# Kernel optimization log

Hardware: AMD Instinct MI355X
Metric: run time of the kernel (lower is better)

Reference implementation:

```python
import jax, jax.numpy as jnp
import numpy as np

B, P, K_NN, HEADS = 4, 2048, 30, 3
N = B * P


def knn_nbr(feat):
    """Per-cloud exact KNN (no self), returns [N, K_NN+1] global neighbor idx, self appended last.
    Matches torch_geometric knn_graph (loop=False) followed by GATConv add_self_loops=True."""
    f = feat.reshape(B, P, -1)
    sq = jnp.sum(f * f, axis=-1)  # [B,P]
    d = sq[:, :, None] + sq[:, None, :] - 2.0 * jnp.einsum('bpc,bqc->bpq', f, f)
    d = d + jnp.eye(P, dtype=f.dtype)[None] * 1e9  # exclude self
    idx = jax.lax.top_k(-d, K_NN)[1]  # [B,P,K_NN] nearest neighbors
    idx = (idx + (jnp.arange(B) * P)[:, None, None]).reshape(N, K_NN)
    return jnp.concatenate([idx, jnp.arange(N)[:, None]], axis=1)  # self-loop last


def gat(xf, nbr, W, a_src, a_dst, bias):
    """PyG GATConv (v1, concat=True, negative_slope=0.2). nbr: [N,K] incoming sources per node."""
    H, F = a_src.shape
    xh = (xf @ W).reshape(N, H, F)
    s = jnp.sum(xh * a_src, axis=-1)  # [N,H] source scores
    t = jnp.sum(xh * a_dst, axis=-1)  # [N,H] target scores
    e = jax.nn.leaky_relu(s[nbr] + t[:, None, :], 0.2)  # [N,K,H]
    alpha = jax.nn.softmax(e, axis=1)  # edge-softmax over incoming edges
    out = jnp.einsum('nkh,nkhf->nhf', alpha, xh[nbr])
    return out.reshape(N, H * F) + bias


def setup_inputs() -> dict:
    key = jax.random.key(0)
    ks = jax.random.split(key, 48)
    w = lambda k, shape: (jax.random.normal(k, shape, jnp.float32) * 0.1)
    H = HEADS
    inp = {
        'x': jax.random.normal(ks[0], (N, 3), jnp.float32),
        'pos': jax.random.normal(ks[1], (N, 3), jnp.float32),
        'batch': (jnp.arange(N) // P).astype(jnp.int32),
        'w1': w(ks[2], (6, 64 * H)), 'as1': w(ks[3], (H, 64)), 'ad1': w(ks[4], (H, 64)), 'b1': w(ks[5], (64 * H,)),
        'ml1w': w(ks[6], (64 * H, 64)), 'ml1b': w(ks[7], (64,)),
        'w2': w(ks[8], (70, 64 * H)), 'as2': w(ks[9], (H, 64)), 'ad2': w(ks[10], (H, 64)), 'b2': w(ks[11], (64 * H,)),
        'ml2w': w(ks[12], (64 * H, 64)), 'ml2b': w(ks[13], (64,)),
        'w3': w(ks[14], (134, 64 * H)), 'as3': w(ks[15], (H, 64)), 'ad3': w(ks[16], (H, 64)), 'b3': w(ks[17], (64 * H,)),
        'ml3w': w(ks[18], (64 * H, 64)), 'ml3b': w(ks[19], (64,)),
        'w4': w(ks[20], (198, 128 * H)), 'as4': w(ks[21], (H, 128)), 'ad4': w(ks[22], (H, 128)), 'b4': w(ks[23], (128 * H,)),
        'ml4w': w(ks[24], (128 * H, 128)), 'ml4b': w(ks[25], (128,)),
        # fe_mlp: 326 -> 1024 -> 1024 (plain last)
        'few1': w(ks[26], (326, 1024)), 'feb1': w(ks[27], (1024,)),
        'few2': w(ks[28], (1024, 1024)), 'feb2': w(ks[29], (1024,)),
        # head mlp: 1350 -> 256 -> 256 -> 128 -> 50
        'mw1': w(ks[30], (1350, 256)), 'mb1': w(ks[31], (256,)),
        'mw2': w(ks[32], (256, 256)), 'mb2': w(ks[33], (256,)),
        'mw3': w(ks[34], (256, 128)), 'mb3': w(ks[35], (128,)),
        'mw4': w(ks[36], (128, 50)), 'mb4': w(ks[37], (50,)),
    }
    return inp


def reference(x, pos, batch,
              w1, as1, ad1, b1, ml1w, ml1b,
              w2, as2, ad2, b2, ml2w, ml2b,
              w3, as3, ad3, b3, ml3w, ml3b,
              w4, as4, ad4, b4, ml4w, ml4b,
              few1, feb1, few2, feb2,
              mw1, mb1, mw2, mb2, mw3, mb3, mw4, mb4):
    x0 = jnp.concatenate([x, pos], axis=-1)  # [N,6]
    nbr = knn_nbr(x0)
    x1 = gat(x0, nbr, w1, as1, ad1, b1) @ ml1w + ml1b  # [N,64]
    nbr = knn_nbr(x1)
    x2 = gat(jnp.concatenate([x0, x1], 1), nbr, w2, as2, ad2, b2) @ ml2w + ml2b
    nbr = knn_nbr(x2)
    x3 = gat(jnp.concatenate([x0, x1, x2], 1), nbr, w3, as3, ad3, b3) @ ml3w + ml3b
    nbr = knn_nbr(x2)  # faithful to source: 4th graph also built from x2
    x4 = gat(jnp.concatenate([x0, x1, x2, x3], 1), nbr, w4, as4, ad4, b4) @ ml4w + ml4b
    link4 = jnp.concatenate([x0, x1, x2, x3, x4], axis=-1)  # [N,326]
    h = jax.nn.relu(link4 @ few1 + feb1) @ few2 + feb2  # [N,1024]
    g = jnp.max(h, axis=0, keepdims=True)  # global feature (dropout=eval identity)
    lg = jnp.concatenate([link4, jnp.broadcast_to(g, (N, h.shape[1]))], axis=1)
    h = jax.nn.relu(lg @ mw1 + mb1)
    h = jax.nn.relu(h @ mw2 + mb2)
    h = jax.nn.relu(h @ mw3 + mb3)
    out = h @ mw4 + mb4
    return jax.nn.log_softmax(out, axis=1)
```

## Files before the change

### kernel.cpp

```cpp
#include <hip/hip_runtime.h>
#include <hip/hip_bf16.h>
#include <hip/amd_detail/amd_hip_vector_types.h>

#define NPTS 8192
#define PP 2048
#define KNN 30
#define KTOT 31
#define HEADS 3
#define LDH 352
#define NSEG 9
#define LDZ 200
#define LDZ4 392

typedef __attribute__((ext_vector_type(8))) short short8;
typedef __attribute__((ext_vector_type(4))) float floatx4;
typedef __attribute__((ext_vector_type(4))) unsigned int uint4_t;
typedef unsigned short ushort_t;
typedef unsigned int uint_t;

__device__ inline ushort_t f2bs(float v) {
    __hip_bfloat16 b = __float2bfloat16(v);
    return *reinterpret_cast<ushort_t*>(&b);
}
__device__ inline float bs2f(ushort_t u) {
    __hip_bfloat16 b = *reinterpret_cast<__hip_bfloat16*>(&u);
    return __bfloat162float(b);
}
__device__ inline void split2(float v, ushort_t& h, ushort_t& l) {
    h = f2bs(v);
    l = f2bs(v - bs2f(h));
}
__device__ inline uint_t fenc(float f) {
    uint_t b = __float_as_uint(f);
    return (b & 0x80000000u) ? ~b : (b | 0x80000000u);
}
__device__ inline float fdec(uint_t e) {
    return __uint_as_float((e & 0x80000000u) ? (e & 0x7FFFFFFFu) : ~e);
}

__global__ void k_build_x0(const float* __restrict__ x, const float* __restrict__ pos,
                           ushort_t* __restrict__ lh, ushort_t* __restrict__ ll) {
    int i = blockIdx.x * blockDim.x + threadIdx.x;
    if (i >= NPTS * 6) return;
    int n = i / 6, c = i % 6;
    float v = (c < 3) ? x[n * 3 + c] : pos[n * 3 + (c - 3)];
    ushort_t h, l; split2(v, h, l);
    lh[(size_t)n * LDH + c] = h;
    ll[(size_t)n * LDH + c] = l;
}

template<int F_>
__global__ __launch_bounds__(128)
void k_combine(const float* __restrict__ w, const float* __restrict__ mlw,
               const float* __restrict__ as_, const float* __restrict__ ad,
               const float* __restrict__ b, const float* __restrict__ mlb,
               float* __restrict__ wc, float* __restrict__ bc, int K_) {
    constexpr int NC = 3 * F_ + 6;
    constexpr int JG = 128 / F_;
    constexpr int RG = 8 / JG;
    int lb = blockIdx.x;
    int h = lb % 3, kb = lb / 3;
    int k0 = kb * 8, KS = min(8, K_ - k0);
    int tid = threadIdx.x;
    int j = tid % F_, rg = tid / F_;
    __shared__ float ws[8][F_];
    __shared__ float ms[32][F_];
    __shared__ float bav[3][F_];
    for (int idx = tid; idx < 8 * F_; idx += 128) {
        int r = idx / F_, f = idx % F_;
        ws[r][f] = (r < KS) ? w[(size_t)(k0 + r) * (3 * F_) + h * F_ + f] : 0.f;
    }
    for (int f = tid; f < F_; f += 128) {
        bav[0][f] = b[h * F_ + f];
        bav[1][f] = as_[h * F_ + f];
        bav[2][f] = ad[h * F_ + f];
    }
    __syncthreads();
    const float* mh = mlw + (size_t)h * F_ * F_;
    float acc[RG] = {};
    float bacc = 0.f;
    for (int f0 = 0; f0 < F_; f0 += 32) {
        for (int idx = tid; idx < 32 * F_; idx += 128) {
            int u = idx / F_, jj = idx % F_;
            ms[u][jj] = mh[(size_t)(f0 + u) * F_ + jj];
        }
        __syncthreads();
#pragma unroll
        for (int u = 0; u < 32; u++) {
            float m = ms[u][j];
#pragma unroll
            for (int r = 0; r < RG; r++)
                acc[r] += ws[rg * RG + r][f0 + u] * m;
            if (rg == 0) bacc += bav[0][f0 + u] * m;
        }
        __syncthreads();
    }
#pragma unroll
    for (int r = 0; r < RG; r++) {
        int k = k0 + rg * RG + r;
        if (k < K_) wc[(size_t)k * NC + h * F_ + j] = acc[r];
    }
    if (kb == 0 && rg == 0)
        atomicAdd(&bc[j], bacc + (h == 0 ? mlb[j] : 0.f));
    if (tid < 16) {
        int r = tid >> 1, sc = tid & 1;
        if (r < KS) {
            float s = 0.f;
#pragma unroll
            for (int f = 0; f < F_; f++) s += ws[r][f] * bav[1 + sc][f];
            wc[(size_t)(k0 + r) * NC + 3 * F_ + sc * 3 + h] = s;
        }
    }
}

__global__ void k_tw1(const float* __restrict__ x, const float* __restrict__ pos,
                      const float* __restrict__ wc, float* __restrict__ z) {
    int t = blockIdx.x * blockDim.x + threadIdx.x;
    if (t >= NPTS * 198) return;
    int n = t / 198, j = t % 198;
    float acc = 0.f;
#pragma unroll
    for (int c = 0; c < 3; c++) {
        acc += x[n * 3 + c] * wc[c * 198 + j];
        acc += pos[n * 3 + c] * wc[(3 + c) * 198 + j];
    }
    z[(size_t)n * LDZ + j] = acc;
}

struct WArgs {
    const float* src[NSEG];
    ushort_t* dst[NSEG];
    int K[NSEG], N[NSEG], Kp[NSEG], t0[NSEG];
};
__global__ void k_wsplit_all(WArgs a) {
    int bt = blockIdx.x;
    int si = 0;
#pragma unroll
    for (int i = 1; i < NSEG; i++) if (bt >= a.t0[i]) si = i;
    int t = bt - a.t0[si];
    int K_ = a.K[si], N_ = a.N[si], Kp = a.Kp[si];
    const float* src = a.src[si];
    ushort_t* dh = a.dst[si];
    ushort_t* dl = dh + (size_t)Kp * N_;
    int tX = (N_ + 31) >> 5;
    int k0 = (t / tX) * 32, n0 = (t % tX) * 32;
    __shared__ float tt[32][33];
    int c = threadIdx.x & 31, r8 = threadIdx.x >> 5;
#pragma unroll
    for (int i = 0; i < 4; i++) {
        int r = r8 + i * 8;
        int k = k0 + r, n = n0 + c;
        tt[r][c] = (k < K_ && n < N_) ? src[(size_t)k * N_ + n] : 0.f;
    }
    __syncthreads();
#pragma unroll
    for (int i = 0; i < 4; i++) {
        int r = r8 + i * 8;
        int n = n0 + r, k = k0 + c;
        if (n < N_) {
            float v = tt[c][r];
            ushort_t h, l; split2(v, h, l);
            dh[(size_t)n * Kp + k] = h;
            dl[(size_t)n * Kp + k] = l;
        }
    }
}

template<int MT, int NT>
__global__ __launch_bounds__(256)
void k_mgemm1(const ushort_t* __restrict__ A, int lda,
              const ushort_t* __restrict__ W, int ldw,
              float* __restrict__ Cf, int ldc,
              ushort_t* __restrict__ Ch, int ldh,
              int Ndim, int K,
              const float* __restrict__ bias1, const float* __restrict__ bias2,
              int relu, int lsm, uint_t* __restrict__ gmax) {
    constexpr int MTW = MT / 64;
    constexpr int NTT = NT / 16;
    __shared__ ushort_t As[2][MT * 40];
    __shared__ ushort_t Bs[2][NT * 40];
    __shared__ uint_t smax[NT];
    int tid = threadIdx.x;
    int w = tid >> 6, lane = tid & 63;
    int quad = lane >> 4, l16 = lane & 15;
    int m0 = blockIdx.x * MT, n0 = blockIdx.y * NT;
    uint4_t pa[MT / 64], pb[NT / 64];
    auto prefetch = [&](int k0) {
#pragma unroll
        for (int rep = 0; rep < MT / 64; rep++) {
            int idx = tid + rep * 256;
            int row = idx >> 2, q = idx & 3;
            pa[rep] = *(const uint4_t*)(A + (size_t)(m0 + row) * lda + k0 + q * 8);
        }
#pragma unroll
        for (int rep = 0; rep < NT / 64; rep++) {
            int idx = tid + rep * 256;
            int row = idx >> 2, q = idx & 3;
            uint4_t v = {0, 0, 0, 0};
            if (n0 + row < Ndim) v = *(const uint4_t*)(W + (size_t)(n0 + row) * ldw + k0 + q * 8);
            pb[rep] = v;
        }
    };
    auto stage = [&](int buf) {
#pragma unroll
        for (int rep = 0; rep < MT / 64; rep++) {
            int idx = tid + rep * 256;
            int row = idx >> 2, q = idx & 3;
            *(uint4_t*)&As[buf][row * 40 + q * 8] = pa[rep];
        }
#pragma unroll
        for (int rep = 0; rep < NT / 64; rep++) {
            int idx = tid + rep * 256;
            int row = idx >> 2, q = idx & 3;
            *(uint4_t*)&Bs[buf][row * 40 + q * 8] = pb[rep];
        }
    };
    if (gmax) {
        for (int idx = tid; idx < NT; idx += 256) smax[idx] = 0u;
    }
    floatx4 acc[MTW][NTT] = {};
    prefetch(0);
    stage(0);
    __syncthreads();
    int cur = 0;
    for (int k0 = 0; k0 < K; k0 += 32) {
        bool more = (k0 + 32 < K);
        if (more) prefetch(k0 + 32);
        short8 ah[MTW];
#pragma unroll
        for (int mt = 0; mt < MTW; mt++) {
            int r = w * (MT / 4) + mt * 16 + l16;
            ah[mt] = *(short8*)&As[cur][r * 40 + quad * 8];
        }
#pragma unroll
        for (int nt = 0; nt < NTT; nt++) {
            int r = nt * 16 + l16;
            short8 bh = *(short8*)&Bs[cur][r * 40 + quad * 8];
#pragma unroll
            for (int mt = 0; mt < MTW; mt++)
                acc[mt][nt] = __builtin_amdgcn_mfma_f32_16x16x32_bf16(ah[mt], bh, acc[mt][nt], 0, 0, 0);
        }
        if (more) stage(cur ^ 1);
        __syncthreads();
        cur ^= 1;
    }
    if (lsm) {
#pragma unroll
        for (int mt = 0; mt < MTW; mt++) {
#pragma unroll
            for (int r = 0; r < 4; r++) {
                float vv[NTT];
                float mrow = -3e38f;
#pragma unroll
                for (int nt = 0; nt < NTT; nt++) {
                    int n = n0 + nt * 16 + l16;
                    float val = (n < Ndim) ? acc[mt][nt][r] + bias1[n] : -3e38f;
                    vv[nt] = val;
                    mrow = fmaxf(mrow, val);
                }
#pragma unroll
                for (int off = 8; off >= 1; off >>= 1)
                    mrow = fmaxf(mrow, __shfl_xor(mrow, off, 64));
                float s = 0.f;
#pragma unroll
                for (int nt = 0; nt < NTT; nt++)
                    if (vv[nt] > -1e38f) s += expf(vv[nt] - mrow);
#pragma unroll
                for (int off = 8; off >= 1; off >>= 1)
                    s += __shfl_xor(s, off, 64);
                float lse = mrow + logf(s);
                int m = m0 + w * (MT / 4) + mt * 16 + quad * 4 + r;
#pragma unroll
                for (int nt = 0; nt < NTT; nt++) {
                    int n = n0 + nt * 16 + l16;
                    if (n < Ndim) Cf[(size_t)m * ldc + n] = vv[nt] - lse;
                }
            }
        }
        return;
    }
    if (gmax) {
#pragma unroll
        for (int mt = 0; mt < MTW; mt++) {
#pragma unroll
            for (int nt = 0; nt < NTT; nt++) {
#pragma unroll
                for (int r = 0; r < 4; r++) {
                    float v = acc[mt][nt][r] + bias1[nt * 16 + l16 + n0];
                    atomicMax(&smax[nt * 16 + l16], fenc(v));
                }
            }
        }
        __syncthreads();
        for (int idx = tid; idx < NT; idx += 256)
            atomicMax(&gmax[n0 + idx], smax[idx]);
        return;
    }
#pragma unroll
    for (int mt = 0; mt < MTW; mt++) {
#pragma unroll
        for (int nt = 0; nt < NTT; nt++) {
#pragma unroll
            for (int r = 0; r < 4; r++) {
                int m = m0 + w * (MT / 4) + mt * 16 + quad * 4 + r;
                int n = n0 + nt * 16 + l16;
                if (n < Ndim) {
                    float v = acc[mt][nt][r];
                    if (bias1) v += bias1[n];
                    if (bias2) v += bias2[n];
                    if (relu && v < 0.f) v = 0.f;
                    if (Cf) Cf[(size_t)m * ldc + n] = v;
                    if (Ch) Ch[(size_t)m * ldh + n] = f2bs(v);
                }
            }
        }
    }
}

__global__ __launch_bounds__(256)
void k_mgemm3(const ushort_t* __restrict__ Ah, const ushort_t* __restrict__ Al, int lda,
              const ushort_t* __restrict__ Wh, const ushort_t* __restrict__ Wl, int ldw,
              float* __restrict__ Cf, int ldc,
              int Ndim, int K) {
    constexpr int NTT = 4;
    __shared__ ushort_t AsH[64 * 40], BsH[64 * 40], AsL[64 * 40], BsL[64 * 40];
    int tid = threadIdx.x;
    int w = tid >> 6, lane = tid & 63;
    int quad = lane >> 4, l16 = lane & 15;
    int m0 = blockIdx.y * 64, n0 = blockIdx.x * 64;
    floatx4 acc[NTT] = {};
    for (int k0 = 0; k0 < K; k0 += 32) {
        {
            int row = tid >> 2, q = tid & 3;
            size_t go = (size_t)(m0 + row) * lda + k0 + q * 8;
            *(uint4_t*)&AsH[row * 40 + q * 8] = *(const uint4_t*)(Ah + go);
            *(uint4_t*)&AsL[row * 40 + q * 8] = *(const uint4_t*)(Al + go);
            uint4_t vh = {0, 0, 0, 0}, vl = {0, 0, 0, 0};
            size_t gw = (size_t)(n0 + row) * ldw + k0 + q * 8;
            if (n0 + row < Ndim) { vh = *(const uint4_t*)(Wh + gw); vl = *(const uint4_t*)(Wl + gw); }
            *(uint4_t*)&BsH[row * 40 + q * 8] = vh;
            *(uint4_t*)&BsL[row * 40 + q * 8] = vl;
        }
        __syncthreads();
        short8 ah, al;
        {
            int r = w * 16 + l16;
            ah = *(short8*)&AsH[r * 40 + quad * 8];
            al = *(short8*)&AsL[r * 40 + quad * 8];
        }
#pragma unroll
        for (int nt = 0; nt < NTT; nt++) {
            int r = nt * 16 + l16;
            short8 bh = *(short8*)&BsH[r * 40 + quad * 8];
            short8 bl = *(short8*)&BsL[r * 40 + quad * 8];
            acc[nt] = __builtin_amdgcn_mfma_f32_16x16x32_bf16(ah, bh, acc[nt], 0, 0, 0);
            acc[nt] = __builtin_amdgcn_mfma_f32_16x16x32_bf16(ah, bl, acc[nt], 0, 0, 0);
            acc[nt] = __builtin_amdgcn_mfma_f32_16x16x32_bf16(al, bh, acc[nt], 0, 0, 0);
        }
        __syncthreads();
    }
#pragma unroll
    for (int nt = 0; nt < NTT; nt++) {
#pragma unroll
        for (int r = 0; r < 4; r++) {
            int m = m0 + w * 16 + quad * 4 + r;
            int n = n0 + nt * 16 + l16;
            if (n < Ndim) Cf[(size_t)m * ldc + n] = acc[nt][r];
        }
    }
}

__global__ __launch_bounds__(256)
void k_mdist(const ushort_t* __restrict__ Lh, const ushort_t* __restrict__ Ll,
             int co, int C, uint_t* __restrict__ keys) {
    __shared__ ushort_t AsH[128 * 40], AsL[128 * 40], BsH[64 * 40], BsL[64 * 40];
    __shared__ float sqa[128], sqb[64];
    int tid = threadIdx.x;
    int w = tid >> 6, lane = tid & 63;
    int quad = lane >> 4, l16 = lane & 15;
    int b = blockIdx.z, cb = b * PP;
    int i0 = blockIdx.y * 128, j0 = blockIdx.x * 64;
    floatx4 acc[2][4] = {};
    float sacc = 0.f;
    for (int k0 = 0; k0 < C; k0 += 32) {
#pragma unroll
        for (int rep = 0; rep < 8; rep++) {
            int d = tid + rep * 256;
            int row = d >> 4, c2 = d & 15;
            size_t gi = ((size_t)(cb + i0 + row) * LDH + co + k0 + c2 * 2) >> 1;
            *(uint_t*)&AsH[row * 40 + c2 * 2] = ((const uint_t*)Lh)[gi];
            *(uint_t*)&AsL[row * 40 + c2 * 2] = ((const uint_t*)Ll)[gi];
        }
#pragma unroll
        for (int rep = 0; rep < 4; rep++) {
            int d = tid + rep * 256;
            int row = d >> 4, c2 = d & 15;
            size_t gi = ((size_t)(cb + j0 + row) * LDH + co + k0 + c2 * 2) >> 1;
            *(uint_t*)&BsH[row * 40 + c2 * 2] = ((const uint_t*)Lh)[gi];
            *(uint_t*)&BsL[row * 40 + c2 * 2] = ((const uint_t*)Ll)[gi];
        }
        __syncthreads();
        if (tid < 128) {
#pragma unroll
            for (int kk = 0; kk < 16; kk++) {
                uint_t ph = *(uint_t*)&AsH[tid * 40 + kk * 2];
                uint_t pl = *(uint_t*)&AsL[tid * 40 + kk * 2];
                float v0 = bs2f((ushort_t)(ph & 0xFFFFu)) + bs2f((ushort_t)(pl & 0xFFFFu));
                sacc += v0 * v0;
                float v1 = bs2f((ushort_t)(ph >> 16)) + bs2f((ushort_t)(pl >> 16));
                sacc += v1 * v1;
            }
        } else if (tid < 192) {
            int row = tid - 128;
#pragma unroll
            for (int kk = 0; kk < 16; kk++) {
                uint_t ph = *(uint_t*)&BsH[row * 40 + kk * 2];
                uint_t pl = *(uint_t*)&BsL[row * 40 + kk * 2];
                float v0 = bs2f((ushort_t)(ph & 0xFFFFu)) + bs2f((ushort_t)(pl & 0xFFFFu));
                sacc += v0 * v0;
                float v1 = bs2f((ushort_t)(ph >> 16)) + bs2f((ushort_t)(pl >> 16));
                sacc += v1 * v1;
            }
        }
        short8 ah[2], al[2];
#pragma unroll
        for (int mt = 0; mt < 2; mt++) {
            int r = w * 32 + mt * 16 + l16;
            ah[mt] = *(short8*)&AsH[r * 40 + quad * 8];
            al[mt] = *(short8*)&AsL[r * 40 + quad * 8];
        }
#pragma unroll
        for (int nt = 0; nt < 4; nt++) {
            int r = nt * 16 + l16;
            short8 bh = *(short8*)&BsH[r * 40 + quad * 8];
            short8 bl = *(short8*)&BsL[r * 40 + quad * 8];
#pragma unroll
            for (int mt = 0; mt < 2; mt++) {
                acc[mt][nt] = __builtin_amdgcn_mfma_f32_16x16x32_bf16(ah[mt], bh, acc[mt][nt], 0, 0, 0);
                acc[mt][nt] = __builtin_amdgcn_mfma_f32_16x16x32_bf16(ah[mt], bl, acc[mt][nt], 0, 0, 0);
                acc[mt][nt] = __builtin_amdgcn_mfma_f32_16x16x32_bf16(al[mt], bh, acc[mt][nt], 0, 0, 0);
            }
        }
        __syncthreads();
    }
    if (tid < 128) sqa[tid] = sacc;
    else if (tid < 192) sqb[tid - 128] = sacc;
    __syncthreads();
#pragma unroll
    for (int mt = 0; mt < 2; mt++) {
#pragma unroll
        for (int nt = 0; nt < 4; nt++) {
#pragma unroll
            for (int r = 0; r < 4; r++) {
                int li = w * 32 + mt * 16 + quad * 4 + r;
                int lj = nt * 16 + l16;
                int il = i0 + li, jl = j0 + lj;
                float dd = sqa[li] + sqb[lj] - 2.f * acc[mt][nt][r];
                dd = (il == jl) ? 3e9f : fmaxf(dd, 0.f);
                uint_t key = (__float_as_uint(dd) & 0xFFFFF800u) | (uint_t)jl;
                __builtin_nontemporal_store(key, &keys[(size_t)(cb + il) * PP + jl]);
            }
        }
    }
}

__global__ __launch_bounds__(256)
void k_topk(const uint_t* __restrict__ keys, int* __restrict__ nbr) {
    int r = blockIdx.x * 4 + (threadIdx.x >> 6);
    int lane = threadIdx.x & 63;
    int base = (r / PP) * PP;
    const uint_t* row = keys + (size_t)r * PP;
    uint_t v[32];
#pragma unroll
    for (int j = 0; j < 8; j++)
        *(uint4_t*)&v[j * 4] = *(const uint4_t*)(row + lane * 4 + j * 256);
    uint_t g[8];
#pragma unroll
    for (int j = 0; j < 8; j++)
        g[j] = min(min(v[j * 4], v[j * 4 + 1]), min(v[j * 4 + 2], v[j * 4 + 3]));
    uint_t lv = g[0];
#pragma unroll
    for (int j = 1; j < 8; j++) lv = min(lv, g[j]);
    for (int sel = 0; sel < KNN; sel++) {
        uint_t bk = lv;
#pragma unroll
        for (int off = 32; off > 0; off >>= 1)
            bk = min(bk, (uint_t)__shfl_xor((int)bk, off, 64));
        uint_t bks = __builtin_amdgcn_readfirstlane(bk);
        if (lane == 0) nbr[r * KTOT + sel] = base + (int)(bks & 0x7FFu);
        int grp = (int)((bks & 0x7FFu) >> 8);
#pragma unroll
        for (int jj = 0; jj < 8; jj++)
            if (grp == jj) {
#pragma unroll
                for (int t = 0; t < 4; t++)
                    v[jj * 4 + t] = (v[jj * 4 + t] == bks) ? 0xFFFFFFFFu : v[jj * 4 + t];
                g[jj] = min(min(v[jj * 4], v[jj * 4 + 1]), min(v[jj * 4 + 2], v[jj * 4 + 3]));
            }
        lv = g[0];
#pragma unroll
        for (int j = 1; j < 8; j++) lv = min(lv, g[j]);
    }
    if (lane == 0) nbr[r * KTOT + KNN] = r;
}

template<int F>
__global__ __launch_bounds__(3 * F)
void k_gat2(const float* __restrict__ z, int ldz,
            const int* __restrict__ nbr,
            const float* __restrict__ bc,
            ushort_t* __restrict__ dh, ushort_t* __restrict__ dl) {
    __shared__ int srcs[KTOT];
    __shared__ float alpha[KTOT * HEADS];
    __shared__ float part[HEADS * F];
    int i = (blockIdx.x & 3) * PP + (blockIdx.x >> 2);
    int tid = threadIdx.x;
    if (tid < KTOT) srcs[tid] = nbr[i * KTOT + tid];
    __syncthreads();
    if (tid < KTOT * HEADS) {
        int k = tid / HEADS, h = tid % HEADS;
        float e = z[(size_t)srcs[k] * ldz + 3 * F + h] + z[(size_t)i * ldz + 3 * F + 3 + h];
        if (e < 0.f) e *= 0.2f;
        alpha[tid] = e;
    }
    __syncthreads();
    if (tid < HEADS) {
        int h = tid;
        float m = -3e38f;
        for (int k = 0; k < KTOT; k++) m = fmaxf(m, alpha[k * HEADS + h]);
        float sum = 0.f;
        for (int k = 0; k < KTOT; k++) {
            float ex = expf(alpha[k * HEADS + h] - m);
            alpha[k * HEADS + h] = ex;
            sum += ex;
        }
        float inv = 1.f / sum;
        for (int k = 0; k < KTOT; k++) alpha[k * HEADS + h] *= inv;
    }
    __syncthreads();
    int h = tid / F, j = tid % F;
    float acc = 0.f;
    for (int k = 0; k < KTOT; k++)
        acc += alpha[k * HEADS + h] * z[(size_t)srcs[k] * ldz + h * F + j];
    part[h * F + j] = acc;
    __syncthreads();
    if (tid < F) {
        float v = part[tid] + part[F + tid] + part[2 * F + tid] + bc[tid];
        ushort_t hi = f2bs(v);
        dh[(size_t)i * LDH + tid] = hi;
        if (dl) dl[(size_t)i * LDH + tid] = f2bs(v - bs2f(hi));
    }
}

__global__ void k_gproj(const uint_t* __restrict__ genc,
                        const float* __restrict__ mw1,
                        const float* __restrict__ mb1,
                        float* __restrict__ gproj) {
    __shared__ float gs[128];
    int kb = blockIdx.x;
    int t = threadIdx.x;
    if (t < 128) gs[t] = fdec(genc[kb * 128 + t]);
    __syncthreads();
    float acc = (kb == 0) ? mb1[t] : 0.f;
    for (int k = 0; k < 128; k++)
        acc += gs[k] * mw1[(size_t)(326 + kb * 128 + k) * 256 + t];
    atomicAdd(&gproj[t], acc);
}

struct WT { ushort_t *h, *l; int kp; };

extern "C" void kernel_launch(void* const* d_in, const int* in_sizes, int n_in,
                              void* d_out, int out_size, void* d_ws, size_t ws_size,
                              hipStream_t stream) {
    (void)in_sizes; (void)n_in; (void)out_size; (void)ws_size;
    const float* x    = (const float*)d_in[0];
    const float* pos  = (const float*)d_in[1];
    const float* w1   = (const float*)d_in[3];
    const float* as1  = (const float*)d_in[4];
    const float* ad1  = (const float*)d_in[5];
    const float* b1   = (const float*)d_in[6];
    const float* ml1w = (const float*)d_in[7];
    const float* ml1b = (const float*)d_in[8];
    const float* w2   = (const float*)d_in[9];
    const float* as2  = (const float*)d_in[10];
    const float* ad2  = (const float*)d_in[11];
    const float* b2   = (const float*)d_in[12];
    const float* ml2w = (const float*)d_in[13];
    const float* ml2b = (const float*)d_in[14];
    const float* w3   = (const float*)d_in[15];
    const float* as3  = (const float*)d_in[16];
    const float* ad3  = (const float*)d_in[17];
    const float* b3   = (const float*)d_in[18];
    const float* ml3w = (const float*)d_in[19];
    const float* ml3b = (const float*)d_in[20];
    const float* w4   = (const float*)d_in[21];
    const float* as4  = (const float*)d_in[22];
    const float* ad4  = (const float*)d_in[23];
    const float* b4   = (const float*)d_in[24];
    const float* ml4w = (const float*)d_in[25];
    const float* ml4b = (const float*)d_in[26];
    const float* few1 = (const float*)d_in[27];
    const float* feb1 = (const float*)d_in[28];
    const float* few2 = (const float*)d_in[29];
    const float* feb2 = (const float*)d_in[30];
    const float* mw1  = (const float*)d_in[31];
    const float* mb1  = (const float*)d_in[32];
    const float* mw2  = (const float*)d_in[33];
    const float* mb2  = (const float*)d_in[34];
    const float* mw3  = (const float*)d_in[35];
    const float* mb3  = (const float*)d_in[36];
    const float* mw4  = (const float*)d_in[37];
    const float* mb4  = (const float*)d_in[38];

    float* Wb = (float*)d_ws;
    size_t off = 0;
    auto alloc = [&](size_t n) { float* p = Wb + off; off += (n + 63) & ~(size_t)63; return p; };

    float*    dist = alloc((size_t)NPTS * PP);
    ushort_t* l4h  = (ushort_t*)alloc((size_t)NPTS * LDH / 2);
    ushort_t* l4l  = (ushort_t*)alloc((size_t)NPTS * LDH / 2);
    uint_t* genc = (uint_t*)alloc(1024);
    float* gproj = alloc(256);
    int*   nbr   = (int*)alloc((size_t)NPTS * KTOT);
    ushort_t* wtpool = (ushort_t*)alloc(1742336);
    float* wc1 = alloc(6 * 198);
    float* wc2 = alloc(70 * 198);
    float* wc3 = alloc(134 * 198);
    float* wc4 = alloc(198 * 390);
    float* bcp = alloc(320);
    float* bc1 = bcp, *bc2 = bcp + 64, *bc3 = bcp + 128, *bc4 = bcp + 192;

    char* d0 = (char*)dist;
    uint_t*   dkey = (uint_t*)dist;
    float*    z    = dist;
    ushort_t* hah  = (ushort_t*)d0;
    ushort_t* bBh  = (ushort_t*)(d0 + (size_t)NPTS * 1024 * 2);
    ushort_t* bAh = (ushort_t*)d0;
    ushort_t* bCh = (ushort_t*)d0;

    hipMemsetAsync(l4h, 0, (size_t)NPTS * LDH * 4, stream);
    hipMemsetAsync(gproj, 0, 256 * 4, stream);
    hipMemsetAsync(genc, 0, 1024 * 4, stream);
    hipMemsetAsync(bcp, 0, 320 * 4, stream);

    k_combine<64><<<1 * 3, 128, 0, stream>>>(w1, ml1w, as1, ad1, b1, ml1b, wc1, bc1, 6);
    k_combine<64><<<9 * 3, 128, 0, stream>>>(w2, ml2w, as2, ad2, b2, ml2b, wc2, bc2, 70);
    k_combine<64><<<17 * 3, 128, 0, stream>>>(w3, ml3w, as3, ad3, b3, ml3b, wc3, bc3, 134);
    k_combine<128><<<25 * 3, 128, 0, stream>>>(w4, ml4w, as4, ad4, b4, ml4b, wc4, bc4, 198);

    WArgs wa;
    WT wt[NSEG];
    {
        const float* srcs[NSEG] = {wc2, wc3, wc4, few1, few2, mw1, mw2, mw3, mw4};
        int Ks[NSEG] = {70, 134, 198, 326, 1024, 326, 256, 256, 128};
        int Ns[NSEG] = {198, 198, 390, 1024, 1024, 256, 256, 128, 50};
        size_t wo = 0; int tiles = 0;
        for (int i = 0; i < NSEG; i++) {
            int kp = (Ks[i] + 31) & ~31;
            wa.src[i] = srcs[i];
            wa.dst[i] = wtpool + wo;
            wa.K[i] = Ks[i]; wa.N[i] = Ns[i]; wa.Kp[i] = kp;
            wa.t0[i] = tiles;
            wt[i] = { wtpool + wo, wtpool + wo + (size_t)kp * Ns[i], kp };
            wo += (size_t)2 * kp * Ns[i];
            tiles += (kp / 32) * ((Ns[i] + 31) / 32);
        }
        k_wsplit_all<<<tiles, 256, 0, stream>>>(wa);
    }
    WT tw2 = wt[0], tw3 = wt[1], tw4 = wt[2], tfe1 = wt[3], tfe2 = wt[4],
       tmw1 = wt[5], tmw2 = wt[6], tmw3 = wt[7], tmw4 = wt[8];

    auto mg3 = [&](const ushort_t* Ah, const ushort_t* Al, int lda, WT t,
                   float* Cf, int ldc, int Nd, int K) {
        dim3 g((Nd + 63) / 64, NPTS / 64);
        k_mgemm3<<<g, 256, 0, stream>>>(Ah, Al, lda, t.h, t.l, t.kp, Cf, ldc, Nd, K);
    };
    auto mg1 = [&](int MT, int NT, const ushort_t* Ah, int lda, WT t,
                   float* Cf, int ldc, ushort_t* Ch, int ldhh,
                   int Nd, int K, const float* bb1, const float* bb2,
                   int relu, int lsm, uint_t* gmax) {
        dim3 g(NPTS / MT, (Nd + NT - 1) / NT);
        if (MT == 128 && NT == 128)
            k_mgemm1<128, 128><<<g, 256, 0, stream>>>(Ah, lda, t.h, t.kp, Cf, ldc, Ch, ldhh, Nd, K,
                bb1, bb2, relu, lsm, gmax);
        else if (MT == 128)
            k_mgemm1<128, 64><<<g, 256, 0, stream>>>(Ah, lda, t.h, t.kp, Cf, ldc, Ch, ldhh, Nd, K,
                bb1, bb2, relu, lsm, gmax);
        else
            k_mgemm1<64, 64><<<g, 256, 0, stream>>>(Ah, lda, t.h, t.kp, Cf, ldc, Ch, ldhh, Nd, K,
                bb1, bb2, relu, lsm, gmax);
    };

    dim3 dgrid(PP / 64, PP / 128, 4);
    k_build_x0<<<(NPTS * 6 + 255) / 256, 256, 0, stream>>>(x, pos, l4h, l4l);

    k_mdist<<<dgrid, 256, 0, stream>>>(l4h, l4l, 0, 6, dkey);
    k_topk<<<NPTS / 4, 256, 0, stream>>>(dkey, nbr);
    k_tw1<<<(NPTS * 198 + 255) / 256, 256, 0, stream>>>(x, pos, wc1, z);
    k_gat2<64><<<NPTS, 192, 0, stream>>>(z, LDZ, nbr, bc1, l4h + 6, l4l + 6);

    k_mdist<<<dgrid, 256, 0, stream>>>(l4h, l4l, 6, 64, dkey);
    k_topk<<<NPTS / 4, 256, 0, stream>>>(dkey, nbr);
    mg3(l4h, l4l, LDH, tw2, z, LDZ, 198, 70);
    k_gat2<64><<<NPTS, 192, 0, stream>>>(z, LDZ, nbr, bc2, l4h + 70, l4l + 70);

    k_mdist<<<dgrid, 256, 0, stream>>>(l4h, l4l, 70, 64, dkey);
    k_topk<<<NPTS / 4, 256, 0, stream>>>(dkey, nbr);
    mg1(64, 64, l4h, LDH, tw3, z, LDZ, nullptr, 0, 198, 134, nullptr, nullptr, 0, 0, nullptr);
    k_gat2<64><<<NPTS, 192, 0, stream>>>(z, LDZ, nbr, bc3, l4h + 134, nullptr);

    mg1(64, 64, l4h, LDH, tw4, z, LDZ4, nullptr, 0, 390, 198, nullptr, nullptr, 0, 0, nullptr);
    k_gat2<128><<<NPTS, 384, 0, stream>>>(z, LDZ4, nbr, bc4, l4h + 198, nullptr);

    mg1(128, 128, l4h, LDH, tfe1, nullptr, 0, hah, 1024, 1024, 326, feb1, nullptr, 1, 0, nullptr);
    mg1(128, 128, hah, 1024, tfe2, nullptr, 0, nullptr, 0, 1024, 1024, feb2, nullptr, 0, 0, genc);
    k_gproj<<<8, 256, 0, stream>>>(genc, mw1, mb1, gproj);

    mg1(128, 64, l4h, LDH, tmw1, nullptr, 0, bAh, 256, 256, 326, nullptr, gproj, 1, 0, nullptr);
    mg1(128, 64, bAh, 256, tmw2, nullptr, 0, bBh, 256, 256, 256, mb2, nullptr, 1, 0, nullptr);
    mg1(64, 64, bBh, 256, tmw3, nullptr, 0, bCh, 128, 128, 256, mb3, nullptr, 1, 0, nullptr);
    mg1(64, 64, bCh, 128, tmw4, (float*)d_out, 50, nullptr, 0, 50, 128, mb4, nullptr, 0, 1, nullptr);
}
```

Measured before the change: 591.7 us.

## Parallelize GAT edge softmax with shuffles and pack multiple nodes per block

The GAT aggregation kernel now computes the per-head edge softmax with 32-lane shuffle reductions instead of three threads looping serially over 31 edges. For F=64 each block handles two nodes. Each thread accumulates two adjacent output features using two independent accumulator chains, and results are written as packed 32-bit bf16 pairs. The F=128 layer now runs with 192 threads per block. The aim is to remove the serial softmax bottleneck and an extra barrier, and to raise work per thread. In exchange, shared memory per block grows and the kernel relies on a split2 helper defined elsewhere in the file.

```diff
diff --git a/kernel.cpp b/kernel.cpp
--- a/kernel.cpp
+++ b/kernel.cpp
@@ -504,51 +504,84 @@
     if (lane == 0) nbr[r * KTOT + KNN] = r;
 }
 
-template<int F>
-__global__ __launch_bounds__(3 * F)
+template<int F, int NN>
+__global__ __launch_bounds__(192)
 void k_gat2(const float* __restrict__ z, int ldz,
             const int* __restrict__ nbr,
             const float* __restrict__ bc,
             ushort_t* __restrict__ dh, ushort_t* __restrict__ dl) {
-    __shared__ int srcs[KTOT];
-    __shared__ float alpha[KTOT * HEADS];
-    __shared__ float part[HEADS * F];
-    int i = (blockIdx.x & 3) * PP + (blockIdx.x >> 2);
+    constexpr int TPN = 3 * F / 2;
+    __shared__ int srcs[NN][KTOT];
+    __shared__ float alpha[NN][96];
+    __shared__ float part[NN][2][F];
     int tid = threadIdx.x;
-    if (tid < KTOT) srcs[tid] = nbr[i * KTOT + tid];
+    if (tid < NN * KTOT) {
+        int u = tid / KTOT, k = tid % KTOT;
+        int t = blockIdx.x * NN + u;
+        int node = (t & 3) * PP + (t >> 2);
+        srcs[u][k] = nbr[node * KTOT + k];
+    }
     __syncthreads();
-    if (tid < KTOT * HEADS) {
-        int k = tid / HEADS, h = tid % HEADS;
-        float e = z[(size_t)srcs[k] * ldz + 3 * F + h] + z[(size_t)i * ldz + 3 * F + 3 + h];
-        if (e < 0.f) e *= 0.2f;
-        alpha[tid] = e;
+    if (tid < NN * 96) {
+        int u = tid / 96, r = tid % 96, h = r >> 5, k = r & 31;
+        int t = blockIdx.x * NN + u;
+        int node = (t & 3) * PP + (t >> 2);
+        float e = -3e38f;
+        if (k < KTOT) {
+            float sv = z[(size_t)srcs[u][k] * ldz + 3 * F + h];
+            float tv = z[(size_t)node * ldz + 3 * F + 3 + h];
+            e = sv + tv;
+            if (e < 0.f) e *= 0.2f;
+        }
+        float m = e;
+#pragma unroll
+        for (int off = 16; off >= 1; off >>= 1)
+            m = fmaxf(m, __shfl_xor(m, off, 32));
+        float ex = (k < KTOT) ? expf(e - m) : 0.f;
+        float s = ex;
+#pragma unroll
+        for (int off = 16; off >= 1; off >>= 1)
+            s += __shfl_xor(s, off, 32);
+        alpha[u][h * 32 + k] = ex / s;
     }
     __syncthreads();
-    if (tid < HEADS) {
-        int h = tid;
-        float m = -3e38f;
-        for (int k = 0; k < KTOT; k++) m = fmaxf(m, alpha[k * HEADS + h]);
-        float sum = 0.f;
-        for (int k = 0; k < KTOT; k++) {
-            float ex = expf(alpha[k * HEADS + h] - m);
-            alpha[k * HEADS + h] = ex;
-            sum += ex;
-        }
-        float inv = 1.f / sum;
-        for (int k = 0; k < KTOT; k++) alpha[k * HEADS + h] *= inv;
-    }
-    __syncthreads();
-    int h = tid / F, j = tid % F;
-    float acc = 0.f;
-    for (int k = 0; k < KTOT; k++)
-        acc += alpha[k * HEADS + h] * z[(size_t)srcs[k] * ldz + h * F + j];
-    part[h * F + j] = acc;
-    __syncthreads();
-    if (tid < F) {
-        float v = part[tid] + part[F + tid] + part[2 * F + tid] + bc[tid];
-        ushort_t hi = f2bs(v);
-        dh[(size_t)i * LDH + tid] = hi;
-        if (dl) dl[(size_t)i * LDH + tid] = f2bs(v - bs2f(hi));
+    {
+        int u = tid / TPN, r = tid % TPN;
+        int h = r / (F / 2), jp = r % (F / 2);
+        const float* zb = z + h * F + jp * 2;
+        float a0x = 0.f, a0y = 0.f, a1x = 0.f, a1y = 0.f;
+#pragma unroll
+        for (int k = 0; k < KTOT; k += 2) {
+            float a = alpha[u][h * 32 + k];
+            const float* p = zb + (size_t)srcs[u][k] * ldz;
+            a0x += a * p[0];
+            a0y += a * p[1];
+            if (k + 1 < KTOT) {
+                float a2 = alpha[u][h * 32 + k + 1];
+                const float* p2 = zb + (size_t)srcs[u][k + 1] * ldz;
+                a1x += a2 * p2[0];
+                a1y += a2 * p2[1];
+            }
+        }
+        float ax = a0x + a1x, ay = a0y + a1y;
+        if (h > 0) {
+            part[u][h - 1][jp * 2] = ax;
+            part[u][h - 1][jp * 2 + 1] = ay;
+        }
+        __syncthreads();
+        if (h == 0) {
+            int t = blockIdx.x * NN + u;
+            int node = (t & 3) * PP + (t >> 2);
+            int j0 = jp * 2;
+            float v0 = ax + part[u][0][j0] + part[u][1][j0] + bc[j0];
+            float v1 = ay + part[u][0][j0 + 1] + part[u][1][j0 + 1] + bc[j0 + 1];
+            ushort_t h0, l0, h1, l1;
+            split2(v0, h0, l0);
+            split2(v1, h1, l1);
+            *(uint_t*)&dh[(size_t)node * LDH + j0] = (uint_t)h0 | ((uint_t)h1 << 16);
+            if (dl)
+                *(uint_t*)&dl[(size_t)node * LDH + j0] = (uint_t)l0 | ((uint_t)l1 << 16);
+        }
     }
 }
 
@@ -697,20 +730,20 @@
     k_mdist<<<dgrid, 256, 0, stream>>>(l4h, l4l, 0, 6, dkey);
     k_topk<<<NPTS / 4, 256, 0, stream>>>(dkey, nbr);
     k_tw1<<<(NPTS * 198 + 255) / 256, 256, 0, stream>>>(x, pos, wc1, z);
-    k_gat2<64><<<NPTS, 192, 0, stream>>>(z, LDZ, nbr, bc1, l4h + 6, l4l + 6);
+    k_gat2<64, 2><<<NPTS / 2, 192, 0, stream>>>(z, LDZ, nbr, bc1, l4h + 6, l4l + 6);
 
     k_mdist<<<dgrid, 256, 0, stream>>>(l4h, l4l, 6, 64, dkey);
     k_topk<<<NPTS / 4, 256, 0, stream>>>(dkey, nbr);
     mg3(l4h, l4l, LDH, tw2, z, LDZ, 198, 70);
-    k_gat2<64><<<NPTS, 192, 0, stream>>>(z, LDZ, nbr, bc2, l4h + 70, l4l + 70);
+    k_gat2<64, 2><<<NPTS / 2, 192, 0, stream>>>(z, LDZ, nbr, bc2, l4h + 70, l4l + 70);
 
     k_mdist<<<dgrid, 256, 0, stream>>>(l4h, l4l, 70, 64, dkey);
     k_topk<<<NPTS / 4, 256, 0, stream>>>(dkey, nbr);
     mg1(64, 64, l4h, LDH, tw3, z, LDZ, nullptr, 0, 198, 134, nullptr, nullptr, 0, 0, nullptr);
-    k_gat2<64><<<NPTS, 192, 0, stream>>>(z, LDZ, nbr, bc3, l4h + 134, nullptr);
+    k_gat2<64, 2><<<NPTS / 2, 192, 0, stream>>>(z, LDZ, nbr, bc3, l4h + 134, nullptr);
 
     mg1(64, 64, l4h, LDH, tw4, z, LDZ4, nullptr, 0, 390, 198, nullptr, nullptr, 0, 0, nullptr);
-    k_gat2<128><<<NPTS, 384, 0, stream>>>(z, LDZ4, nbr, bc4, l4h + 198, nullptr);
+    k_gat2<128, 1><<<NPTS, 192, 0, stream>>>(z, LDZ4, nbr, bc4, l4h + 198, nullptr);
 
     mg1(128, 128, l4h, LDH, tfe1, nullptr, 0, hah, 1024, 1024, 326, feb1, nullptr, 1, 0, nullptr);
     mg1(128, 128, hah, 1024, tfe2, nullptr, 0, nullptr, 0, 1024, 1024, feb2, nullptr, 0, 0, genc);
```

Result: faster. 569.6 us (-3.7%).
